# Performance work log

Measured on AMD Instinct MI355X. Metric: run time of the kernel, lower is better.

## Reference

```python
import jax, jax.numpy as jnp
import numpy as np

T, B = 96, 64
D_M, D_MA, D_MV, D_G = 1024, 100, 512, 512
H = D_G // 2  # LSTM hidden per direction


def _ln2(r):
    # torch nn.LayerNorm((seq_len, feature_dim), elementwise_affine=False) applied to [B,T,F]:
    # normalize each batch element over all (T,F) entries. r here is [T,B,F].
    m = r.mean(axis=(0, 2), keepdims=True)
    v = r.var(axis=(0, 2), keepdims=True)
    return (r - m) / jnp.sqrt(v + 1e-5)


def _lstm_dir(x, Wih, Whh, bih, bhh, reverse):
    # x: [T,B,Din]; Wih: [4H,Din]; Whh: [4H,H]. torch gate order: i,f,g,o.
    xg = jnp.einsum('tbd,gd->tbg', x, Wih) + bih + bhh
    def step(carry, xt):
        h, c = carry
        g = xt + h @ Whh.T
        i, f, gg, o = jnp.split(g, 4, axis=-1)
        c = jax.nn.sigmoid(f) * c + jax.nn.sigmoid(i) * jnp.tanh(gg)
        h = jax.nn.sigmoid(o) * jnp.tanh(c)
        return (h, c), h
    z = jnp.zeros((x.shape[1], Whh.shape[1]), x.dtype)
    _, hs = jax.lax.scan(step, (z, z), xg, reverse=reverse)
    return hs  # [T,B,H], time-aligned for both directions


def _bilstm_layer(x, Wf, Uf, bf, cf, Wb, Ub, bb, cb):
    return jnp.concatenate([_lstm_dir(x, Wf, Uf, bf, cf, False),
                            _lstm_dir(x, Wb, Ub, bb, cb, True)], axis=-1)


def _graphify(feat):
    # simple_batch_graphify with full lengths: concat per-dialog utterance features,
    # batch-major -> [B*T, D]
    return jnp.transpose(feat, (1, 0, 2)).reshape(feat.shape[1] * feat.shape[0], -1)


def setup_inputs():
    key = jax.random.key(0)
    ks = jax.random.split(key, 32)
    f = lambda k, s: jax.random.normal(k, s, dtype=jnp.float32)
    w = lambda k, s: f(k, s) * 0.05
    inp = {
        'r1': f(ks[0], (T, B, D_M)), 'r2': f(ks[1], (T, B, D_M)),
        'r3': f(ks[2], (T, B, D_M)), 'r4': f(ks[3], (T, B, D_M)),
        'U_a': f(ks[4], (T, B, D_MA)), 'U_v': f(ks[5], (T, B, D_MV)),
        'seq_lengths': jnp.full((B,), T, dtype=jnp.int32),
        'W_a': w(ks[6], (D_G, D_MA)), 'b_a': jnp.zeros((D_G,), jnp.float32),
        'W_v': w(ks[7], (D_G, D_MV)), 'b_v': jnp.zeros((D_G,), jnp.float32),
        'W_l': w(ks[8], (D_G, D_M)),  'b_l': jnp.zeros((D_G,), jnp.float32),
    }
    # 2-layer bidirectional LSTM: layer0 in=D_G, layer1 in=2H=D_G, hidden H per direction
    i = 9
    for layer, din in ((0, D_G), (1, 2 * H)):
        for d in ('f', 'b'):
            inp[f'Wih{layer}{d}'] = w(ks[i], (4 * H, din)); i += 1
            inp[f'Whh{layer}{d}'] = w(ks[i], (4 * H, H)); i += 1
            inp[f'bih{layer}{d}'] = jnp.zeros((4 * H,), jnp.float32)
            inp[f'bhh{layer}{d}'] = jnp.zeros((4 * H,), jnp.float32)
    return inp


def reference(r1, r2, r3, r4, U_a, U_v, seq_lengths,
              W_a, b_a, W_v, b_v, W_l, b_l,
              Wih0f, Whh0f, bih0f, bhh0f, Wih0b, Whh0b, bih0b, bhh0b,
              Wih1f, Whh1f, bih1f, bhh1f, Wih1b, Whh1b, bih1b, bhh1b):
    # norm_strategy == 'LN2'
    r1, r2, r3, r4 = _ln2(r1), _ln2(r2), _ln2(r3), _ln2(r4)
    U = (r1 + r2 + r3 + r4) / 4.0  # [T,B,D_M]

    # base_model == 'LSTM', multi_modal, av_using_lstm=False (eval: dropout inactive)
    emotions_a = U_a @ W_a.T + b_a            # [T,B,D_G]
    emotions_v = U_v @ W_v.T + b_v            # [T,B,D_G]
    Ul = U @ W_l.T + b_l                      # [T,B,D_G]
    h0 = _bilstm_layer(Ul, Wih0f, Whh0f, bih0f, bhh0f, Wih0b, Whh0b, bih0b, bhh0b)
    emotions_l = _bilstm_layer(h0, Wih1f, Whh1f, bih1f, bhh1f, Wih1b, Whh1b, bih1b, bhh1b)

    features_a = _graphify(emotions_a)        # [B*T, D_G]
    features_v = _graphify(emotions_v)        # [B*T, D_G]
    features_l = _graphify(emotions_l)        # [B*T, 2H=D_G]
    return jnp.concatenate([features_a, features_v, features_l], axis=-1)  # [B*T, 3*D_G]
```

## Files before the change

kernel.cpp:

```cpp
#include <hip/hip_runtime.h>
#include <hip/hip_bf16.h>
#include <cstddef>

typedef __bf16 bf16_t;
typedef __bf16 bf16x8 __attribute__((ext_vector_type(8)));
typedef __bf16 bf16x4 __attribute__((ext_vector_type(4)));
typedef float f32x4 __attribute__((ext_vector_type(4)));
typedef unsigned int u32x4 __attribute__((ext_vector_type(4)));

#define T_LEN 96
#define BATCH 64
#define DM 1024
#define NTB 6144

__global__ __launch_bounds__(256) void ln_stats_kernel(
    const float* __restrict__ r1, const float* __restrict__ r2,
    const float* __restrict__ r3, const float* __restrict__ r4,
    float* __restrict__ stats)
{
    const int i = blockIdx.x >> 6, b = blockIdx.x & 63;
    const float* r = (i == 0) ? r1 : (i == 1) ? r2 : (i == 2) ? r3 : r4;
    float s = 0.f, ss = 0.f;
    for (int t = 0; t < T_LEN; ++t) {
        float4 v = ((const float4*)(r + (size_t)(t * BATCH + b) * DM))[threadIdx.x];
        s  += v.x + v.y + v.z + v.w;
        ss += v.x * v.x + v.y * v.y + v.z * v.z + v.w * v.w;
    }
    __shared__ float sh[512];
    sh[threadIdx.x] = s; sh[256 + threadIdx.x] = ss;
    __syncthreads();
    for (int off = 128; off > 0; off >>= 1) {
        if (threadIdx.x < off) {
            sh[threadIdx.x] += sh[threadIdx.x + off];
            sh[256 + threadIdx.x] += sh[256 + threadIdx.x + off];
        }
        __syncthreads();
    }
    if (threadIdx.x == 0) {
        const float inv = 1.0f / (float)(T_LEN * DM);
        float mean = sh[0] * inv;
        float var  = sh[256] * inv - mean * mean;
        stats[blockIdx.x * 2 + 0] = mean;
        stats[blockIdx.x * 2 + 1] = rsqrtf(var + 1e-5f);
    }
}

__global__ __launch_bounds__(256) void compute_u_kernel(
    const float* __restrict__ r1, const float* __restrict__ r2,
    const float* __restrict__ r3, const float* __restrict__ r4,
    const float* __restrict__ stats, bf16_t* __restrict__ U)
{
    const int idx4 = blockIdx.x * 256 + threadIdx.x;
    const int b = (idx4 >> 8) & 63;
    const float m0 = stats[(0 * 64 + b) * 2], s0 = stats[(0 * 64 + b) * 2 + 1];
    const float m1 = stats[(1 * 64 + b) * 2], s1 = stats[(1 * 64 + b) * 2 + 1];
    const float m2 = stats[(2 * 64 + b) * 2], s2 = stats[(2 * 64 + b) * 2 + 1];
    const float m3 = stats[(3 * 64 + b) * 2], s3 = stats[(3 * 64 + b) * 2 + 1];
    float4 a = ((const float4*)r1)[idx4];
    float4 c = ((const float4*)r2)[idx4];
    float4 d = ((const float4*)r3)[idx4];
    float4 e = ((const float4*)r4)[idx4];
    bf16x4 o;
    o[0] = (bf16_t)(0.25f * ((a.x - m0) * s0 + (c.x - m1) * s1 + (d.x - m2) * s2 + (e.x - m3) * s3));
    o[1] = (bf16_t)(0.25f * ((a.y - m0) * s0 + (c.y - m1) * s1 + (d.y - m2) * s2 + (e.y - m3) * s3));
    o[2] = (bf16_t)(0.25f * ((a.z - m0) * s0 + (c.z - m1) * s1 + (d.z - m2) * s2 + (e.z - m3) * s3));
    o[3] = (bf16_t)(0.25f * ((a.w - m0) * s0 + (c.w - m1) * s1 + (d.w - m2) * s2 + (e.w - m3) * s3));
    ((bf16x4*)U)[idx4] = o;
}

__global__ __launch_bounds__(256) void cast_pad_kernel(
    const float* __restrict__ src, bf16_t* __restrict__ dst,
    int rows, int K, int Kpad)
{
    int idx = blockIdx.x * 256 + threadIdx.x;
    if (idx >= rows * Kpad) return;
    int r = idx / Kpad;
    int k = idx - r * Kpad;
    float v = (k < K) ? src[(size_t)r * K + k] : 0.f;
    dst[idx] = (bf16_t)v;
}

__global__ __launch_bounds__(256) void wpk_pack_kernel(
    const float* __restrict__ whh, bf16_t* __restrict__ dst)
{
    int i = blockIdx.x * 256 + threadIdx.x;
    int e = i & 7, lane = (i >> 3) & 63, fid = (i >> 9) & 63, wv = i >> 15;
    int kq = fid & 7, gt = (fid >> 3) & 3, jf = fid >> 5;
    int nrow = gt * 256 + wv * 32 + jf * 16 + (lane & 15);
    int k = kq * 32 + (lane >> 4) * 8 + e;
    dst[i] = (bf16_t)whh[nrow * 256 + k];
}

#define GLDP 40
__global__ __launch_bounds__(256) void gemm_bt_kernel(
    const bf16_t* __restrict__ A, const bf16_t* __restrict__ W,
    const float* __restrict__ bias0, const float* __restrict__ bias1,
    int K, float* __restrict__ outF, bf16_t* __restrict__ outB,
    int ldo, int mode)
{
    __shared__ bf16_t As[128 * GLDP];
    __shared__ bf16_t Bs[128 * GLDP];
    const int tid = threadIdx.x;
    const int lane = tid & 63;
    const int wid = tid >> 6;
    const int q = lane >> 4, l15 = lane & 15;
    const int wr = (wid >> 1) * 64, wc = (wid & 1) * 64;
    const size_t br = (size_t)blockIdx.y * 128;
    const size_t bc = (size_t)blockIdx.x * 128;

    const int r0 = tid >> 2;
    const int r1 = r0 + 64;
    const int k0 = (tid & 3) * 8;

    f32x4 acc[4][4] = {};

    for (int kt = 0; kt < K; kt += 32) {
        bf16x8 a0 = *(const bf16x8*)(A + (br + r0) * K + kt + k0);
        bf16x8 a1 = *(const bf16x8*)(A + (br + r1) * K + kt + k0);
        bf16x8 w0 = *(const bf16x8*)(W + (bc + r0) * K + kt + k0);
        bf16x8 w1 = *(const bf16x8*)(W + (bc + r1) * K + kt + k0);
        if (kt) __syncthreads();
        *(bf16x8*)(As + r0 * GLDP + k0) = a0;
        *(bf16x8*)(As + r1 * GLDP + k0) = a1;
        *(bf16x8*)(Bs + r0 * GLDP + k0) = w0;
        *(bf16x8*)(Bs + r1 * GLDP + k0) = w1;
        __syncthreads();
        bf16x8 bfr[4];
        #pragma unroll
        for (int j = 0; j < 4; ++j)
            bfr[j] = *(const bf16x8*)(Bs + (wc + j * 16 + l15) * GLDP + q * 8);
        #pragma unroll
        for (int i = 0; i < 4; ++i) {
            bf16x8 afr = *(const bf16x8*)(As + (wr + i * 16 + l15) * GLDP + q * 8);
            #pragma unroll
            for (int j = 0; j < 4; ++j)
                acc[i][j] = __builtin_amdgcn_mfma_f32_16x16x32_bf16(afr, bfr[j], acc[i][j], 0, 0, 0);
        }
    }

    #pragma unroll
    for (int j = 0; j < 4; ++j) {
        int col = (int)bc + wc + j * 16 + l15;
        float bv = bias0[col];
        if (bias1) bv += bias1[col];
        #pragma unroll
        for (int i = 0; i < 4; ++i) {
            int rowb = (int)br + wr + i * 16 + q * 4;
            if (mode == 2) {
                int t = rowb >> 6, b = rowb & 63;
                int bg = b >> 4, q2 = (b >> 2) & 3;
                int gt = col >> 8, hcol = col & 255;
                int wv2 = hcol >> 5, jf = (hcol >> 4) & 1, jj = col & 15;
                float4 o4;
                o4.x = acc[i][j][0] + bv; o4.y = acc[i][j][1] + bv;
                o4.z = acc[i][j][2] + bv; o4.w = acc[i][j][3] + bv;
                *(float4*)(outF + (((size_t)bg * 96 + t) * 16384)
                                 + wv2 * 2048 + jf * 1024 + gt * 256
                                 + (q2 * 16 + jj) * 4) = o4;
            } else {
                #pragma unroll
                for (int rr = 0; rr < 4; ++rr) {
                    int row = rowb + rr;
                    float v = acc[i][j][rr] + bv;
                    if (mode == 0) {
                        outB[(size_t)row * ldo + col] = (bf16_t)v;
                    } else {
                        int orow = (row & 63) * T_LEN + (row >> 6);
                        outF[(size_t)orow * ldo + col] = v;
                    }
                }
            }
        }
    }
}

#define RVN 44
#define RLN 18
#define HB_P 264

__device__ __forceinline__ float sig_f(float x) {
    return __builtin_amdgcn_rcpf(1.0f + __expf(-x));
}
__device__ __forceinline__ float tanh_f(float x) {
    return 1.0f - 2.0f * __builtin_amdgcn_rcpf(1.0f + __expf(2.0f * x));
}

__global__ __launch_bounds__(512, 2) void lstm_batch_kernel(
    const float* __restrict__ xg2f, const float* __restrict__ xg2b,
    const bf16_t* __restrict__ wpkf, const bf16_t* __restrict__ wpkb,
    bf16_t* __restrict__ hall)
{
    __shared__ bf16_t wlds[8 * RLN * 512];
    __shared__ bf16_t hband[16 * HB_P];

    const int tid = threadIdx.x;
    const int dir = blockIdx.x >> 2, bg = blockIdx.x & 3;
    const int wv = tid >> 6, lane = tid & 63, q = lane >> 4, l15 = lane & 15;
    const int b0 = bg * 16;

    const float* xgw = (dir ? xg2b : xg2f) + (size_t)bg * 96 * 16384 + wv * 2048 + lane * 4;
    const bf16_t* wp = (dir ? wpkb : wpkf) + ((size_t)wv * 4096 + lane) * 8;

    u32x4 wreg[RVN];
    #pragma unroll
    for (int f = 0; f < RVN; ++f)
        wreg[f] = *(const u32x4*)(wp + (size_t)f * 512);
    #pragma unroll
    for (int f = 0; f < RVN; ++f)
        asm volatile("" : "+v"(wreg[f]));
    #pragma unroll
    for (int f = 0; f < RLN; ++f) {
        bf16x8 v = *(const bf16x8*)(wp + (size_t)(RVN + f) * 512);
        *(bf16x8*)(wlds + (((wv * RLN + f) << 9) + lane * 8)) = v;
    }

    float cstA[4] = {0.f, 0.f, 0.f, 0.f};
    float cstB[4] = {0.f, 0.f, 0.f, 0.f};

    for (int s = 0; s < 96; ++s) {
        const int t = dir ? (95 - s) : s;
        const float* xgt = xgw + (size_t)t * 16384;
        f32x4 xga[4];
        #pragma unroll
        for (int gt = 0; gt < 4; ++gt) xga[gt] = *(const f32x4*)(xgt + gt * 256);

        f32x4 acc[4] = {};
        if (s > 0) {
            #pragma unroll
            for (int kq = 0; kq < 8; ++kq) {
                bf16x8 af = *(const bf16x8*)(hband + l15 * HB_P + kq * 32 + q * 8);
                #pragma unroll
                for (int gt = 0; gt < 4; ++gt)
                    acc[gt] = __builtin_amdgcn_mfma_f32_16x16x32_bf16(
                        af, __builtin_bit_cast(bf16x8, wreg[gt * 8 + kq]), acc[gt], 0, 0, 0);
            }
        }
        u32x4 sv0 = *(const volatile u32x4*)(wp + (size_t)62 * 512);
        u32x4 sv1 = *(const volatile u32x4*)(wp + (size_t)63 * 512);
        f32x4 xgb[4];
        #pragma unroll
        for (int gt = 0; gt < 4; ++gt) xgb[gt] = *(const f32x4*)(xgt + 1024 + gt * 256);

        float hvA[4], hvB[4];
        #pragma unroll
        for (int rr = 0; rr < 4; ++rr) {
            float ai  = acc[0][rr] + xga[0][rr];
            float af_ = acc[1][rr] + xga[1][rr];
            float ag  = acc[2][rr] + xga[2][rr];
            float ao  = acc[3][rr] + xga[3][rr];
            float iv = sig_f(ai), fv = sig_f(af_);
            float gv = tanh_f(ag), ov = sig_f(ao);
            cstA[rr] = (s == 0) ? (iv * gv) : (fv * cstA[rr] + iv * gv);
            hvA[rr] = ov * tanh_f(cstA[rr]);
        }

        f32x4 accB[4] = {};
        if (s > 0) {
            #pragma unroll
            for (int kq = 0; kq < 8; ++kq) {
                bf16x8 af = *(const bf16x8*)(hband + l15 * HB_P + kq * 32 + q * 8);
                #pragma unroll
                for (int gt = 0; gt < 4; ++gt) {
                    const int fid = 32 + gt * 8 + kq;
                    bf16x8 bw;
                    if (fid < RVN)
                        bw = __builtin_bit_cast(bf16x8, wreg[fid]);
                    else if (fid < RVN + RLN)
                        bw = *(const bf16x8*)(wlds + (((wv * RLN + (fid - RVN)) << 9) + lane * 8));
                    else
                        bw = __builtin_bit_cast(bf16x8, (fid == 62) ? sv0 : sv1);
                    accB[gt] = __builtin_amdgcn_mfma_f32_16x16x32_bf16(af, bw, accB[gt], 0, 0, 0);
                }
            }
        }
        #pragma unroll
        for (int rr = 0; rr < 4; ++rr) {
            float ai  = accB[0][rr] + xgb[0][rr];
            float af_ = accB[1][rr] + xgb[1][rr];
            float ag  = accB[2][rr] + xgb[2][rr];
            float ao  = accB[3][rr] + xgb[3][rr];
            float iv = sig_f(ai), fv = sig_f(af_);
            float gv = tanh_f(ag), ov = sig_f(ao);
            cstB[rr] = (s == 0) ? (iv * gv) : (fv * cstB[rr] + iv * gv);
            hvB[rr] = ov * tanh_f(cstB[rr]);
        }

        __syncthreads();
        #pragma unroll
        for (int rr = 0; rr < 4; ++rr) {
            hband[(q * 4 + rr) * HB_P + wv * 32 + l15]      = (bf16_t)hvA[rr];
            hband[(q * 4 + rr) * HB_P + wv * 32 + 16 + l15] = (bf16_t)hvB[rr];
        }
        __syncthreads();
        {
            const int bl = tid >> 5, c8 = (tid & 31) * 8;
            bf16x8 v = *(const bf16x8*)(hband + bl * HB_P + c8);
            *(bf16x8*)(hall + (((size_t)t * 64 + b0 + bl) << 9) + dir * 256 + c8) = v;
        }
    }
}

__global__ __launch_bounds__(256) void out_expand_kernel(
    const bf16_t* __restrict__ hall, float* __restrict__ out)
{
    const int t = blockIdx.x;
    const int b = threadIdx.x >> 2, seg = threadIdx.x & 3;
    const bf16_t* src = hall + (((size_t)t * 64 + b) << 9) + seg * 128;
    float* dst = out + ((size_t)b * 96 + t) * 1536 + seg * 128;
    #pragma unroll
    for (int i = 0; i < 16; ++i) {
        bf16x8 v = ((const bf16x8*)src)[i];
        float4 lo, hi;
        lo.x = (float)v[0]; lo.y = (float)v[1]; lo.z = (float)v[2]; lo.w = (float)v[3];
        hi.x = (float)v[4]; hi.y = (float)v[5]; hi.z = (float)v[6]; hi.w = (float)v[7];
        ((float4*)dst)[2 * i]     = lo;
        ((float4*)dst)[2 * i + 1] = hi;
    }
}

extern "C" void kernel_launch(void* const* d_in, const int* in_sizes, int n_in,
                              void* d_out, int out_size, void* d_ws, size_t ws_size,
                              hipStream_t stream)
{
    const float* r1 = (const float*)d_in[0];
    const float* r2 = (const float*)d_in[1];
    const float* r3 = (const float*)d_in[2];
    const float* r4 = (const float*)d_in[3];
    const float* U_a = (const float*)d_in[4];
    const float* U_v = (const float*)d_in[5];
    const float* W_a = (const float*)d_in[7];
    const float* b_a = (const float*)d_in[8];
    const float* W_v = (const float*)d_in[9];
    const float* b_v = (const float*)d_in[10];
    const float* W_l = (const float*)d_in[11];
    const float* b_l = (const float*)d_in[12];
    const float* Wih0f = (const float*)d_in[13];
    const float* Whh0f = (const float*)d_in[14];
    const float* bih0f = (const float*)d_in[15];
    const float* bhh0f = (const float*)d_in[16];
    const float* Wih0b = (const float*)d_in[17];
    const float* Whh0b = (const float*)d_in[18];
    const float* bih0b = (const float*)d_in[19];
    const float* bhh0b = (const float*)d_in[20];
    const float* Wih1f = (const float*)d_in[21];
    const float* Whh1f = (const float*)d_in[22];
    const float* bih1f = (const float*)d_in[23];
    const float* bhh1f = (const float*)d_in[24];
    const float* Wih1b = (const float*)d_in[25];
    const float* Whh1b = (const float*)d_in[26];
    const float* bih1b = (const float*)d_in[27];
    const float* bhh1b = (const float*)d_in[28];
    float* out = (float*)d_out;

    char* wsb = (char*)d_ws;
    size_t off = 0;
    auto alloc = [&](size_t bytes) -> void* {
        void* p = wsb + off;
        off = (off + bytes + 255) & ~(size_t)255;
        return p;
    };
    float*  stats   = (float*)alloc(512 * sizeof(float));
    bf16_t* Ub      = (bf16_t*)alloc((size_t)NTB * 1024 * 2);
    bf16_t* Uab     = (bf16_t*)alloc((size_t)NTB * 128 * 2);
    bf16_t* Wab     = (bf16_t*)alloc((size_t)512 * 128 * 2);
    bf16_t* Uvb     = (bf16_t*)alloc((size_t)NTB * 512 * 2);
    bf16_t* Wvb     = (bf16_t*)alloc((size_t)512 * 512 * 2);
    bf16_t* Wlb     = (bf16_t*)alloc((size_t)512 * 1024 * 2);
    bf16_t* Wih0fb  = (bf16_t*)alloc((size_t)1024 * 512 * 2);
    bf16_t* Wih0bb  = (bf16_t*)alloc((size_t)1024 * 512 * 2);
    bf16_t* Wih1fb  = (bf16_t*)alloc((size_t)1024 * 512 * 2);
    bf16_t* Wih1bb  = (bf16_t*)alloc((size_t)1024 * 512 * 2);
    bf16_t* Ulb     = (bf16_t*)alloc((size_t)NTB * 512 * 2);
    float*  xgpf    = (float*)alloc((size_t)NTB * 1024 * 4);
    float*  xgpb    = (float*)alloc((size_t)NTB * 1024 * 4);
    bf16_t* wrb0f   = (bf16_t*)alloc((size_t)8 * 64 * 64 * 8 * 2);
    bf16_t* wrb0b   = (bf16_t*)alloc((size_t)8 * 64 * 64 * 8 * 2);
    bf16_t* wrb1f   = (bf16_t*)alloc((size_t)8 * 64 * 64 * 8 * 2);
    bf16_t* wrb1b   = (bf16_t*)alloc((size_t)8 * 64 * 64 * 8 * 2);
    bf16_t* hall0   = (bf16_t*)alloc((size_t)96 * 64 * 512 * 2);
    bf16_t* hall1   = (bf16_t*)alloc((size_t)96 * 64 * 512 * 2);

    ln_stats_kernel<<<256, 256, 0, stream>>>(r1, r2, r3, r4, stats);
    compute_u_kernel<<<NTB * 1024 / 4 / 256, 256, 0, stream>>>(r1, r2, r3, r4, stats, Ub);

    cast_pad_kernel<<<NTB * 128 / 256, 256, 0, stream>>>(U_a, Uab, NTB, 100, 128);
    cast_pad_kernel<<<512 * 128 / 256, 256, 0, stream>>>(W_a, Wab, 512, 100, 128);
    cast_pad_kernel<<<NTB * 512 / 256, 256, 0, stream>>>(U_v, Uvb, NTB, 512, 512);
    cast_pad_kernel<<<512 * 512 / 256, 256, 0, stream>>>(W_v, Wvb, 512, 512, 512);
    cast_pad_kernel<<<512 * 1024 / 256, 256, 0, stream>>>(W_l, Wlb, 512, 1024, 1024);
    cast_pad_kernel<<<1024 * 512 / 256, 256, 0, stream>>>(Wih0f, Wih0fb, 1024, 512, 512);
    cast_pad_kernel<<<1024 * 512 / 256, 256, 0, stream>>>(Wih0b, Wih0bb, 1024, 512, 512);
    cast_pad_kernel<<<1024 * 512 / 256, 256, 0, stream>>>(Wih1f, Wih1fb, 1024, 512, 512);
    cast_pad_kernel<<<1024 * 512 / 256, 256, 0, stream>>>(Wih1b, Wih1bb, 1024, 512, 512);

    wpk_pack_kernel<<<1024, 256, 0, stream>>>(Whh0f, wrb0f);
    wpk_pack_kernel<<<1024, 256, 0, stream>>>(Whh0b, wrb0b);
    wpk_pack_kernel<<<1024, 256, 0, stream>>>(Whh1f, wrb1f);
    wpk_pack_kernel<<<1024, 256, 0, stream>>>(Whh1b, wrb1b);

    gemm_bt_kernel<<<dim3(4, 48), 256, 0, stream>>>(Uab, Wab, b_a, nullptr, 128, out, nullptr, 1536, 1);
    gemm_bt_kernel<<<dim3(4, 48), 256, 0, stream>>>(Uvb, Wvb, b_v, nullptr, 512, out + 512, nullptr, 1536, 1);
    gemm_bt_kernel<<<dim3(4, 48), 256, 0, stream>>>(Ub, Wlb, b_l, nullptr, 1024, nullptr, Ulb, 512, 0);
    gemm_bt_kernel<<<dim3(8, 48), 256, 0, stream>>>(Ulb, Wih0fb, bih0f, bhh0f, 512, xgpf, nullptr, 0, 2);
    gemm_bt_kernel<<<dim3(8, 48), 256, 0, stream>>>(Ulb, Wih0bb, bih0b, bhh0b, 512, xgpb, nullptr, 0, 2);
    lstm_batch_kernel<<<8, 512, 0, stream>>>(xgpf, xgpb, wrb0f, wrb0b, hall0);
    gemm_bt_kernel<<<dim3(8, 48), 256, 0, stream>>>(hall0, Wih1fb, bih1f, bhh1f, 512, xgpf, nullptr, 0, 2);
    gemm_bt_kernel<<<dim3(8, 48), 256, 0, stream>>>(hall0, Wih1bb, bih1b, bhh1b, 512, xgpb, nullptr, 0, 2);
    lstm_batch_kernel<<<8, 512, 0, stream>>>(xgpf, xgpb, wrb1f, wrb1b, hall1);
    out_expand_kernel<<<96, 256, 0, stream>>>(hall1, out + 1024);
}
```

Before: 1.232 ms.

## Hold LSTM recurrent weights in AGPRs and stream more fragments from global

Moves the 32 register-resident recurrent-weight fragments into accumulation registers (AGPRs) and feeds them to MFMA through inline asm. It reorders the packed weight layout so fragments are interleaved by gate, and streams 14 fragments per step from global (L2) instead of 2. The aim is to free VGPRs and change the register/LDS/global split of the weight matrix in the latency-bound recurrent loop. In exchange it adds more global traffic per step, plus manual s_nop hazard padding that could be wrong or costly.

```diff
diff --git a/kernel.cpp b/kernel.cpp
--- a/kernel.cpp
+++ b/kernel.cpp
@@ -85,7 +85,7 @@
 {
     int i = blockIdx.x * 256 + threadIdx.x;
     int e = i & 7, lane = (i >> 3) & 63, fid = (i >> 9) & 63, wv = i >> 15;
-    int kq = fid & 7, gt = (fid >> 3) & 3, jf = fid >> 5;
+    int jf = fid >> 5, kq = (fid >> 2) & 7, gt = fid & 3;
     int nrow = gt * 256 + wv * 32 + jf * 16 + (lane & 15);
     int k = kq * 32 + (lane >> 4) * 8 + e;
     dst[i] = (bf16_t)whh[nrow * 256 + k];
@@ -174,7 +174,7 @@
     }
 }
 
-#define RVN 44
+#define RAN 32
 #define RLN 18
 #define HB_P 264
 
@@ -201,16 +201,15 @@
     const float* xgw = (dir ? xg2b : xg2f) + (size_t)bg * 96 * 16384 + wv * 2048 + lane * 4;
     const bf16_t* wp = (dir ? wpkb : wpkf) + ((size_t)wv * 4096 + lane) * 8;
 
-    u32x4 wreg[RVN];
+    u32x4 wa[RAN];
     #pragma unroll
-    for (int f = 0; f < RVN; ++f)
-        wreg[f] = *(const u32x4*)(wp + (size_t)f * 512);
-    #pragma unroll
-    for (int f = 0; f < RVN; ++f)
-        asm volatile("" : "+v"(wreg[f]));
+    for (int f = 0; f < RAN; ++f) {
+        wa[f] = *(const u32x4*)(wp + (size_t)f * 512);
+        asm volatile("" : "+a"(wa[f]));
+    }
     #pragma unroll
     for (int f = 0; f < RLN; ++f) {
-        bf16x8 v = *(const bf16x8*)(wp + (size_t)(RVN + f) * 512);
+        bf16x8 v = *(const bf16x8*)(wp + (size_t)(RAN + f) * 512);
         *(bf16x8*)(wlds + (((wv * RLN + f) << 9) + lane * 8)) = v;
     }
 
@@ -223,6 +222,10 @@
         f32x4 xga[4];
         #pragma unroll
         for (int gt = 0; gt < 4; ++gt) xga[gt] = *(const f32x4*)(xgt + gt * 256);
+        u32x4 sv[14];
+        #pragma unroll
+        for (int i = 0; i < 7; ++i)
+            sv[i] = *(const volatile u32x4*)(wp + (size_t)(RAN + RLN + i) * 512);
 
         f32x4 acc[4] = {};
         if (s > 0) {
@@ -231,15 +234,20 @@
                 bf16x8 af = *(const bf16x8*)(hband + l15 * HB_P + kq * 32 + q * 8);
                 #pragma unroll
                 for (int gt = 0; gt < 4; ++gt)
-                    acc[gt] = __builtin_amdgcn_mfma_f32_16x16x32_bf16(
-                        af, __builtin_bit_cast(bf16x8, wreg[gt * 8 + kq]), acc[gt], 0, 0, 0);
+                    asm volatile("v_mfma_f32_16x16x32_bf16 %0, %1, %2, %0"
+                                 : "+v"(acc[gt]) : "v"(af), "a"(wa[kq * 4 + gt]));
             }
         }
-        u32x4 sv0 = *(const volatile u32x4*)(wp + (size_t)62 * 512);
-        u32x4 sv1 = *(const volatile u32x4*)(wp + (size_t)63 * 512);
+        #pragma unroll
+        for (int i = 7; i < 14; ++i)
+            sv[i] = *(const volatile u32x4*)(wp + (size_t)(RAN + RLN + i) * 512);
         f32x4 xgb[4];
         #pragma unroll
         for (int gt = 0; gt < 4; ++gt) xgb[gt] = *(const f32x4*)(xgt + 1024 + gt * 256);
+
+        if (s > 0)
+            asm volatile("s_nop 7\n\ts_nop 7\n\ts_nop 7"
+                         : "+v"(acc[0]), "+v"(acc[1]), "+v"(acc[2]), "+v"(acc[3]));
 
         float hvA[4], hvB[4];
         #pragma unroll
@@ -261,14 +269,12 @@
                 bf16x8 af = *(const bf16x8*)(hband + l15 * HB_P + kq * 32 + q * 8);
                 #pragma unroll
                 for (int gt = 0; gt < 4; ++gt) {
-                    const int fid = 32 + gt * 8 + kq;
+                    const int c = kq * 4 + gt;
                     bf16x8 bw;
-                    if (fid < RVN)
-                        bw = __builtin_bit_cast(bf16x8, wreg[fid]);
-                    else if (fid < RVN + RLN)
-                        bw = *(const bf16x8*)(wlds + (((wv * RLN + (fid - RVN)) << 9) + lane * 8));
+                    if (c < RLN)
+                        bw = *(const bf16x8*)(wlds + (((wv * RLN + c) << 9) + lane * 8));
                     else
-                        bw = __builtin_bit_cast(bf16x8, (fid == 62) ? sv0 : sv1);
+                        bw = __builtin_bit_cast(bf16x8, sv[c - RLN]);
                     accB[gt] = __builtin_amdgcn_mfma_f32_16x16x32_bf16(af, bw, accB[gt], 0, 0, 0);
                 }
             }
```

After: 1.674 ms. 1.36x slower.
